# Performance work log

Hardware: AMD Instinct MI355X
Metric: run time of the kernel (lower is better)

The kernel has to match this reference:

```python
import jax, jax.numpy as jnp
import numpy as np

WS = 8  # window size (module uses window_sizes as a scalar)


def setup_inputs() -> dict:
    key = jax.random.key(0)
    ks = jax.random.split(key, 4)
    b, c, h, w = 4, 128, 256, 256
    x = jax.random.normal(ks[0], (b, c, h, w), jnp.float32)
    w_qkv = jax.random.normal(ks[1], (3 * c, c), jnp.float32) * (1.0 / np.sqrt(c))
    w_dw = jax.random.normal(ks[2], (3 * c, 1, 3, 3), jnp.float32) * (1.0 / 3.0)
    w_proj = jax.random.normal(ks[3], (c, c), jnp.float32) * (1.0 / np.sqrt(c))
    temperature = jnp.ones((1, 1, 1), jnp.float32)
    return {"x": x, "w_qkv": w_qkv, "w_dw": w_dw, "w_proj": w_proj,
            "temperature": temperature}


def _window(t, ws):
    # b c (h dh) (w dw) -> b (h w) (dh dw) c
    b, c, H, W = t.shape
    t = t.reshape(b, c, H // ws, ws, W // ws, ws)
    return t.transpose(0, 2, 4, 3, 5, 1).reshape(b, (H // ws) * (W // ws), ws * ws, c)


def _unwindow(t, ws, H, W):
    # b (h w) (dh dw) c -> b c (h dh) (w dw)
    b = t.shape[0]
    c = t.shape[-1]
    t = t.reshape(b, H // ws, W // ws, ws, ws, c)
    return t.transpose(0, 5, 1, 3, 2, 4).reshape(b, c, H, W)


def reference(x, w_qkv, w_dw, w_proj, temperature):
    b, c, H, W = x.shape
    ws = WS
    sh = -ws // 2  # = -(ws//2) for even ws, matching torch.roll shifts
    x_ = jnp.roll(x, (sh, sh), axis=(2, 3))
    # 1x1 conv c -> 3c
    qkv = jnp.einsum('oc,bchw->bohw', w_qkv, x_)
    # depthwise 3x3, padding 1
    qkv = jax.lax.conv_general_dilated(
        qkv, w_dw, window_strides=(1, 1), padding=[(1, 1), (1, 1)],
        dimension_numbers=('NCHW', 'OIHW', 'NCHW'), feature_group_count=3 * c)
    q, k, v = jnp.split(qkv, 3, axis=1)
    q = _window(q, ws)  # [b, nW, ws*ws, c]
    k = _window(k, ws)
    v = _window(v, ws)
    # L2-normalize along channel dim (torch F.normalize, eps=1e-12)
    q = q / jnp.maximum(jnp.linalg.norm(q, axis=-1, keepdims=True), 1e-12)
    k = k / jnp.maximum(jnp.linalg.norm(k, axis=-1, keepdims=True), 1e-12)
    # channel-wise attention: [b, nW, c, c]
    attn = jnp.einsum('bnpc,bnpd->bncd', q, k) * temperature.reshape(())
    attn = jax.nn.relu(attn)
    out = jnp.einsum('bnpc,bncd->bnpd', v, attn)  # [b, nW, ws*ws, c]
    out = _unwindow(out, ws, H, W)
    out = jnp.roll(out, (ws // 2, ws // 2), axis=(2, 3))
    y = jnp.einsum('oc,bchw->bohw', w_proj, out)
    return (y, attn)
```

## Files before the change

kernel.cpp:

```cpp
#include <hip/hip_runtime.h>
#include <hip/hip_bf16.h>

constexpr int NB = 4;
constexpr int CC = 128;
constexpr int HW = 65536;

using bf16x8 = __attribute__((ext_vector_type(8))) short;
using f32x4  = __attribute__((ext_vector_type(4))) float;

__device__ __forceinline__ unsigned short f2bf(float f) {
  unsigned u = __builtin_bit_cast(unsigned, f);
  u += 0x7FFFu + ((u >> 16) & 1u);
  return (unsigned short)(u >> 16);
}
__device__ __forceinline__ float bf2f(unsigned short s) {
  return __builtin_bit_cast(float, (unsigned)s << 16);
}

__device__ __forceinline__ void halo_decomp(int idx, int& ch, int& r, int& c) {
  ch = idx / 30;
  int rem = idx - ch * 30;
  r = rem / 3;
  c = rem - r * 3;
}
__device__ __forceinline__ uint4 halo_load_one(const __hip_bfloat16* __restrict__ base,
                                               int ih0, int iw0, int idx) {
  int ch, r, c;
  halo_decomp(idx, ch, r, c);
  int ii = ih0 - 1 + r, j0 = iw0 - 8 + c * 8;
  uint4 v = {0u, 0u, 0u, 0u};
  if ((unsigned)ii < 256u && (unsigned)j0 <= 248u)
    v = *(const uint4*)(base + (((size_t)ch) << 16) + (ii << 8) + j0);
  return v;
}
__device__ __forceinline__ void halo_store_one(unsigned short* __restrict__ halo,
                                               int idx, uint4 v) {
  int ch, r, c;
  halo_decomp(idx, ch, r, c);
  unsigned short* hrow = halo + ch * 168 + r * 16;
  if (c == 1) *(uint4*)hrow = v;
  else if (c == 0) hrow[9] = (unsigned short)(v.w >> 16);
  else hrow[8] = (unsigned short)(v.x & 0xFFFFu);
}

__device__ __forceinline__ void dw_row(const unsigned short* __restrict__ halo,
                                       const float* __restrict__ wd,
                                       int ch, int pr, float* __restrict__ outv) {
#pragma unroll
  for (int pc = 0; pc < 8; ++pc) outv[pc] = 0.f;
#pragma unroll
  for (int kr = 0; kr < 3; ++kr) {
    const unsigned short* hrow = halo + ch * 168 + (pr + kr) * 16;
    uint4 rw = *(const uint4*)hrow;
    float rv[10];
    rv[0] = bf2f((unsigned short)(rw.x & 0xFFFFu));
    rv[1] = bf2f((unsigned short)(rw.x >> 16));
    rv[2] = bf2f((unsigned short)(rw.y & 0xFFFFu));
    rv[3] = bf2f((unsigned short)(rw.y >> 16));
    rv[4] = bf2f((unsigned short)(rw.z & 0xFFFFu));
    rv[5] = bf2f((unsigned short)(rw.z >> 16));
    rv[6] = bf2f((unsigned short)(rw.w & 0xFFFFu));
    rv[7] = bf2f((unsigned short)(rw.w >> 16));
    rv[8] = bf2f(hrow[8]);
    rv[9] = bf2f(hrow[9]);
#pragma unroll
    for (int s = 0; s < 3; ++s) {
      float wv = wd[kr * 3 + s];
#pragma unroll
      for (int pc = 0; pc < 8; ++pc) {
        int m = pc + s - 1;
        float xv = (m < 0) ? rv[9] : rv[m];
        outv[pc] = fmaf(wv, xv, outv[pc]);
      }
    }
  }
}

__global__ __launch_bounds__(256) void k_qkv_mfma(const float* __restrict__ x,
                                                  const float* __restrict__ wq,
                                                  __hip_bfloat16* __restrict__ qkv) {
  __shared__ unsigned short x_s[128 * 136];

  int blk = blockIdx.x;
  int b = blk >> 9, i = (blk >> 1) & 255, jh = blk & 1;
  int j0 = jh << 7;
  int si = (i + 4) & 255;
  int t = threadIdx.x;

  {
    int c0 = (t & 63) << 1;
    int jb = (t >> 6) << 5;
    const float* xr0 = x + (((size_t)(b * CC + c0)) << 16) + (si << 8);
    const float* xr1 = xr0 + HW;
#pragma unroll
    for (int u = 0; u < 8; ++u) {
      int jj = jb + (u << 2);
      int sj = j0 + jj + 4;
      float v0[4], v1[4];
      if (sj + 3 <= 255) {
        *(float4*)v0 = *(const float4*)(xr0 + sj);
        *(float4*)v1 = *(const float4*)(xr1 + sj);
      } else {
#pragma unroll
        for (int e = 0; e < 4; ++e) {
          int s = (sj + e) & 255;
          v0[e] = xr0[s];
          v1[e] = xr1[s];
        }
      }
#pragma unroll
      for (int e = 0; e < 4; ++e) {
        unsigned pk = (unsigned)f2bf(v0[e]) | ((unsigned)f2bf(v1[e]) << 16);
        *(unsigned*)&x_s[(jj + e) * 136 + c0] = pk;
      }
    }
  }
  __syncthreads();

  int w = t >> 6;
  int lane = t & 63;
  int col = lane & 15;
  int kg = lane >> 4;

#pragma unroll 1
  for (int oi = 0; oi < 3; ++oi) {
    int m0 = oi * 128 + w * 32;
    bf16x8 afr[2][4];
#pragma unroll
    for (int mt = 0; mt < 2; ++mt) {
      const float* wr = wq + (m0 + mt * 16 + col) * CC + kg * 8;
#pragma unroll
      for (int ks = 0; ks < 4; ++ks) {
        float wa[4], wb[4];
        *(float4*)wa = *(const float4*)(wr + ks * 32);
        *(float4*)wb = *(const float4*)(wr + ks * 32 + 4);
        bf16x8 f;
#pragma unroll
        for (int e = 0; e < 4; ++e) {
          f[e] = (short)f2bf(wa[e]);
          f[e + 4] = (short)f2bf(wb[e]);
        }
        afr[mt][ks] = f;
      }
    }
#pragma unroll 1
    for (int n = 0; n < 8; ++n) {
      int px = n * 16 + col;
      f32x4 acc0 = {0.f, 0.f, 0.f, 0.f};
      f32x4 acc1 = {0.f, 0.f, 0.f, 0.f};
#pragma unroll
      for (int ks = 0; ks < 4; ++ks) {
        bf16x8 bfr = *(const bf16x8*)&x_s[px * 136 + ks * 32 + kg * 8];
        acc0 = __builtin_amdgcn_mfma_f32_16x16x32_bf16(afr[0][ks], bfr, acc0, 0, 0, 0);
        acc1 = __builtin_amdgcn_mfma_f32_16x16x32_bf16(afr[1][ks], bfr, acc1, 0, 0, 0);
      }
      int j = j0 + n * 16 + col;
#pragma unroll
      for (int r = 0; r < 4; ++r) {
        int och0 = m0 + kg * 4 + r;
        int och1 = m0 + 16 + kg * 4 + r;
        int g0 = och0 >> 7, c0 = och0 & 127;
        int g1 = och1 >> 7, c1 = och1 & 127;
        qkv[(((size_t)((g0 * NB + b) * CC + c0)) << 16) + (i << 8) + j] =
            __float2bfloat16(acc0[r]);
        qkv[(((size_t)((g1 * NB + b) * CC + c1)) << 16) + (i << 8) + j] =
            __float2bfloat16(acc1[r]);
      }
    }
  }
}

__global__ __launch_bounds__(256) void k_attn(const __hip_bfloat16* __restrict__ qkv,
                                              const float* __restrict__ wdw,
                                              const float* __restrict__ temp_p,
                                              float* __restrict__ attn_out) {
  __shared__ unsigned short halo_s[128 * 168];
  __shared__ unsigned short q_t[128][72];
  __shared__ unsigned short k_t[128][72];
  __shared__ float sumsq_s[2][64];

  int blk = blockIdx.x;
  int b = blk >> 10, n = blk & 1023;
  int ih0 = (n >> 5) << 3, iw0 = (n & 31) << 3;
  int t = threadIdx.x;
  int ch_l = t & 15, grp = t >> 4;
  int pr = grp & 7, contrib = grp >> 3;
  float tau = temp_p[0];
  const __hip_bfloat16* qbase = qkv + (((size_t)(b * CC)) << 16);
  const __hip_bfloat16* kbase = qkv + (((size_t)((NB + b) * CC)) << 16);

#pragma unroll
  for (int it = 0; it < 15; ++it) {
    int idx = it * 256 + t;
    halo_store_one(halo_s, idx, halo_load_one(qbase, ih0, iw0, idx));
  }
  __syncthreads();

  uint4 kpre[15];
#pragma unroll
  for (int it = 0; it < 15; ++it)
    kpre[it] = halo_load_one(kbase, ih0, iw0, it * 256 + t);

  float outv[4][8];
  float ssq[8];
#pragma unroll
  for (int pc = 0; pc < 8; ++pc) ssq[pc] = 0.f;
#pragma unroll
  for (int it = 0; it < 4; ++it) {
    int ch = ((contrib + 2 * it) << 4) + ch_l;
    float wd[9];
#pragma unroll
    for (int kk = 0; kk < 9; ++kk) wd[kk] = wdw[ch * 9 + kk];
    dw_row(halo_s, wd, ch, pr, outv[it]);
#pragma unroll
    for (int pc = 0; pc < 8; ++pc) ssq[pc] = fmaf(outv[it][pc], outv[it][pc], ssq[pc]);
  }
#pragma unroll
  for (int pc = 0; pc < 8; ++pc) {
    float s = ssq[pc];
    s += __shfl_xor(s, 1);
    s += __shfl_xor(s, 2);
    s += __shfl_xor(s, 4);
    s += __shfl_xor(s, 8);
    ssq[pc] = s;
  }
  if (ch_l == 0) {
#pragma unroll
    for (int pc = 0; pc < 8; ++pc) sumsq_s[contrib][pr * 8 + pc] = ssq[pc];
  }
  __syncthreads();

#pragma unroll
  for (int it = 0; it < 15; ++it) halo_store_one(halo_s, it * 256 + t, kpre[it]);

  {
    float psv[8];
#pragma unroll
    for (int pc = 0; pc < 8; ++pc) {
      float s = sumsq_s[0][pr * 8 + pc] + sumsq_s[1][pr * 8 + pc];
      psv[pc] = 1.f / fmaxf(sqrtf(s), 1e-12f);
    }
#pragma unroll
    for (int it = 0; it < 4; ++it) {
      int ch = ((contrib + 2 * it) << 4) + ch_l;
      unsigned short o8[8];
#pragma unroll
      for (int pc = 0; pc < 8; ++pc) o8[pc] = f2bf(outv[it][pc] * psv[pc]);
      *(uint4*)&q_t[ch][pr * 8] = *(const uint4*)o8;
    }
  }
  __syncthreads();

#pragma unroll
  for (int pc = 0; pc < 8; ++pc) ssq[pc] = 0.f;
#pragma unroll
  for (int it = 0; it < 4; ++it) {
    int ch = ((contrib + 2 * it) << 4) + ch_l;
    float wd[9];
#pragma unroll
    for (int kk = 0; kk < 9; ++kk) wd[kk] = wdw[(CC + ch) * 9 + kk];
    dw_row(halo_s, wd, ch, pr, outv[it]);
#pragma unroll
    for (int pc = 0; pc < 8; ++pc) ssq[pc] = fmaf(outv[it][pc], outv[it][pc], ssq[pc]);
  }
#pragma unroll
  for (int pc = 0; pc < 8; ++pc) {
    float s = ssq[pc];
    s += __shfl_xor(s, 1);
    s += __shfl_xor(s, 2);
    s += __shfl_xor(s, 4);
    s += __shfl_xor(s, 8);
    ssq[pc] = s;
  }
  if (ch_l == 0) {
#pragma unroll
    for (int pc = 0; pc < 8; ++pc) sumsq_s[contrib][pr * 8 + pc] = ssq[pc];
  }
  __syncthreads();

  {
    float psv[8];
#pragma unroll
    for (int pc = 0; pc < 8; ++pc) {
      float s = sumsq_s[0][pr * 8 + pc] + sumsq_s[1][pr * 8 + pc];
      psv[pc] = tau / fmaxf(sqrtf(s), 1e-12f);
    }
#pragma unroll
    for (int it = 0; it < 4; ++it) {
      int ch = ((contrib + 2 * it) << 4) + ch_l;
      unsigned short o8[8];
#pragma unroll
      for (int pc = 0; pc < 8; ++pc) o8[pc] = f2bf(outv[it][pc] * psv[pc]);
      *(uint4*)&k_t[ch][pr * 8] = *(const uint4*)o8;
    }
  }
  __syncthreads();

  int wv = t >> 6, lane = t & 63;
  int col = lane & 15, kg = lane >> 4;
  int c0 = wv * 32;
  bf16x8 afr[2][2];
#pragma unroll
  for (int mt = 0; mt < 2; ++mt)
#pragma unroll
    for (int ks = 0; ks < 2; ++ks)
      afr[mt][ks] = *(const bf16x8*)&q_t[c0 + mt * 16 + col][ks * 32 + kg * 8];
  float* ao = attn_out + ((size_t)blk << 14);
#pragma unroll
  for (int dt = 0; dt < 8; ++dt) {
    bf16x8 b0 = *(const bf16x8*)&k_t[dt * 16 + col][kg * 8];
    bf16x8 b1 = *(const bf16x8*)&k_t[dt * 16 + col][32 + kg * 8];
    f32x4 a0 = {0.f, 0.f, 0.f, 0.f};
    f32x4 a1 = {0.f, 0.f, 0.f, 0.f};
    a0 = __builtin_amdgcn_mfma_f32_16x16x32_bf16(afr[0][0], b0, a0, 0, 0, 0);
    a0 = __builtin_amdgcn_mfma_f32_16x16x32_bf16(afr[0][1], b1, a0, 0, 0, 0);
    a1 = __builtin_amdgcn_mfma_f32_16x16x32_bf16(afr[1][0], b0, a1, 0, 0, 0);
    a1 = __builtin_amdgcn_mfma_f32_16x16x32_bf16(afr[1][1], b1, a1, 0, 0, 0);
#pragma unroll
    for (int r = 0; r < 4; ++r) {
      ao[((c0 + kg * 4 + r) << 7) + dt * 16 + col] = fmaxf(a0[r], 0.f);
      ao[((c0 + 16 + kg * 4 + r) << 7) + dt * 16 + col] = fmaxf(a1[r], 0.f);
    }
  }
}

__device__ __forceinline__ int at_addr(int d, int cbyte) {
  int a = d * 272 + cbyte;
  return a ^ (((d >> 2) & 7) << 4);
}

__global__ __launch_bounds__(256) void k_pv(const __hip_bfloat16* __restrict__ qkv,
                                            const float* __restrict__ wdw,
                                            const float* __restrict__ attn,
                                            __hip_bfloat16* __restrict__ out_win) {
  __shared__ unsigned short halo_s[128 * 168];
  __shared__ unsigned short v_t[64][136];

  int blk = blockIdx.x;
  int b = blk >> 10, n = blk & 1023;
  int ih0 = (n >> 5) << 3, iw0 = (n & 31) << 3;
  int t = threadIdx.x;
  int ch_l = t & 15, grp = t >> 4;
  int pr = grp & 7, contrib = grp >> 3;
  const __hip_bfloat16* vbase = qkv + (((size_t)((2 * NB + b) * CC)) << 16);

#pragma unroll
  for (int it = 0; it < 15; ++it) {
    int idx = it * 256 + t;
    halo_store_one(halo_s, idx, halo_load_one(vbase, ih0, iw0, idx));
  }
  __syncthreads();

  const float* ab = attn + ((size_t)blk << 14);
  float4 apre[8][2];
#pragma unroll
  for (int it = 0; it < 8; ++it) {
    int idx = it * 256 + t;
    int d4 = idx & 31, cp = idx >> 5;
    const float* ar = ab + ((2 * cp) << 7) + 4 * d4;
    apre[it][0] = *(const float4*)ar;
    apre[it][1] = *(const float4*)(ar + 128);
  }

#pragma unroll
  for (int it = 0; it < 4; ++it) {
    int ch = ((contrib + 2 * it) << 4) + ch_l;
    float wd[9];
#pragma unroll
    for (int kk = 0; kk < 9; ++kk) wd[kk] = wdw[(2 * CC + ch) * 9 + kk];
    float outv[8];
    dw_row(halo_s, wd, ch, pr, outv);
#pragma unroll
    for (int pc = 0; pc < 8; ++pc) v_t[pr * 8 + pc][ch] = f2bf(outv[pc]);
  }
  __syncthreads();

  unsigned short* a_t = halo_s;
#pragma unroll
  for (int it = 0; it < 8; ++it) {
    int idx = it * 256 + t;
    int d4 = idx & 31, cp = idx >> 5;
    float lo[4], hi[4];
    *(float4*)lo = apre[it][0];
    *(float4*)hi = apre[it][1];
#pragma unroll
    for (int e = 0; e < 4; ++e) {
      unsigned pk = (unsigned)f2bf(lo[e]) | ((unsigned)f2bf(hi[e]) << 16);
      *(unsigned*)((char*)a_t + at_addr(4 * d4 + e, 4 * cp)) = pk;
    }
  }
  __syncthreads();

  int wv = t >> 6, lane = t & 63;
  int col = lane & 15, kg = lane >> 4;
  f32x4 acc[8];
#pragma unroll
  for (int dt = 0; dt < 8; ++dt) acc[dt] = {0.f, 0.f, 0.f, 0.f};
#pragma unroll
  for (int ks = 0; ks < 4; ++ks) {
    bf16x8 va = *(const bf16x8*)&v_t[wv * 16 + col][ks * 32 + kg * 8];
#pragma unroll
    for (int dt = 0; dt < 8; ++dt) {
      bf16x8 bf = *(const bf16x8*)((const char*)a_t +
                                   at_addr(dt * 16 + col, (ks * 32 + kg * 8) * 2));
      acc[dt] = __builtin_amdgcn_mfma_f32_16x16x32_bf16(va, bf, acc[dt], 0, 0, 0);
    }
  }
  __hip_bfloat16* ow = out_win + ((size_t)blk << 13);
#pragma unroll
  for (int dt = 0; dt < 8; ++dt)
#pragma unroll
    for (int r = 0; r < 4; ++r)
      ow[((wv * 16 + kg * 4 + r) << 7) + dt * 16 + col] = __float2bfloat16(acc[dt][r]);
}

__global__ __launch_bounds__(256) void k_proj_mfma(const __hip_bfloat16* __restrict__ out_win,
                                                   const float* __restrict__ wp,
                                                   float* __restrict__ y) {
  __shared__ unsigned short w_s[128 * 136];

  int t = threadIdx.x;
  {
    int och = t >> 1, ch0 = (t & 1) << 6;
    const float* wr = wp + och * CC + ch0;
#pragma unroll
    for (int u = 0; u < 32; ++u) {
      float2 v = *(const float2*)(wr + 2 * u);
      unsigned pk = (unsigned)f2bf(v.x) | ((unsigned)f2bf(v.y) << 16);
      *(unsigned*)&w_s[och * 136 + ch0 + 2 * u] = pk;
    }
  }
  __syncthreads();

  int w = t >> 6, lane = t & 63;
  int col = lane & 15, kg = lane >> 4;
  int bn = blockIdx.x * 4 + w;
  int b = bn >> 10, n = bn & 1023;
  const __hip_bfloat16* ob = out_win + ((size_t)bn << 13);

  bf16x8 afr[8][4];
#pragma unroll
  for (int mt = 0; mt < 8; ++mt)
#pragma unroll
    for (int ks = 0; ks < 4; ++ks)
      afr[mt][ks] = *(const bf16x8*)&w_s[(mt * 16 + col) * 136 + ks * 32 + kg * 8];

#pragma unroll 1
  for (int nt = 0; nt < 4; ++nt) {
    int p = nt * 16 + col;
    bf16x8 bfr[4];
#pragma unroll
    for (int ks = 0; ks < 4; ++ks)
      bfr[ks] = *(const bf16x8*)(ob + p * CC + ks * 32 + kg * 8);
    int i_f = (((n >> 5) << 3) + (p >> 3) + 4) & 255;
    int j_f = (((n & 31) << 3) + (p & 7) + 4) & 255;
    float* yp = y + (((size_t)b * CC) << 16) + (i_f << 8) + j_f;
#pragma unroll
    for (int mt = 0; mt < 8; ++mt) {
      f32x4 acc = {0.f, 0.f, 0.f, 0.f};
#pragma unroll
      for (int ks = 0; ks < 4; ++ks)
        acc = __builtin_amdgcn_mfma_f32_16x16x32_bf16(afr[mt][ks], bfr[ks], acc, 0, 0, 0);
#pragma unroll
      for (int r = 0; r < 4; ++r) {
        int och = mt * 16 + kg * 4 + r;
        yp[(size_t)och << 16] = acc[r];
      }
    }
  }
}

extern "C" void kernel_launch(void* const* d_in, const int* in_sizes, int n_in,
                              void* d_out, int out_size, void* d_ws, size_t ws_size,
                              hipStream_t stream) {
  const float* x = (const float*)d_in[0];
  const float* w_qkv = (const float*)d_in[1];
  const float* w_dw = (const float*)d_in[2];
  const float* w_proj = (const float*)d_in[3];
  const float* temp = (const float*)d_in[4];
  float* y = (float*)d_out;
  float* attn = (float*)d_out + (size_t)NB * CC * HW;

  __hip_bfloat16* qkv = (__hip_bfloat16*)d_ws;
  __hip_bfloat16* out_win = (__hip_bfloat16*)d_ws;

  k_qkv_mfma<<<2048, 256, 0, stream>>>(x, w_qkv, qkv);
  k_attn<<<4096, 256, 0, stream>>>(qkv, w_dw, temp, attn);
  k_pv<<<4096, 256, 0, stream>>>(qkv, w_dw, attn, out_win);
  k_proj_mfma<<<1024, 256, 0, stream>>>(out_win, w_proj, y);
}
```

Measured before the change: 676.8 us.

## Fuse attention, PV and projection kernels into one per-window kernel

Merges k_attn, k_pv and k_proj_mfma into a single kernel. The ReLU'd attention matrix stays in registers and goes to LDS for the PV matmul, instead of being written to global memory and read back. The windowed output also stays in LDS for the projection, which removes the out_win round trip and two kernel launches. The projection weights are now read from global memory and converted to bf16 per block rather than staged once per block in LDS. The change also adds a block-index remap and a launch_bounds occupancy hint, and raises register pressure because the attention accumulators and prefetched V stay live.

```diff
diff --git a/kernel.cpp b/kernel.cpp
--- a/kernel.cpp
+++ b/kernel.cpp
@@ -170,16 +170,19 @@
   }
 }
 
-__global__ __launch_bounds__(256) void k_attn(const __hip_bfloat16* __restrict__ qkv,
-                                              const float* __restrict__ wdw,
-                                              const float* __restrict__ temp_p,
-                                              float* __restrict__ attn_out) {
+__global__ __launch_bounds__(256, 2) void k_fused(const __hip_bfloat16* __restrict__ qkv,
+                                                  const float* __restrict__ wdw,
+                                                  const float* __restrict__ temp_p,
+                                                  const float* __restrict__ wp,
+                                                  float* __restrict__ attn_out,
+                                                  float* __restrict__ y) {
   __shared__ unsigned short halo_s[128 * 168];
   __shared__ unsigned short q_t[128][72];
   __shared__ unsigned short k_t[128][72];
   __shared__ float sumsq_s[2][64];
 
-  int blk = blockIdx.x;
+  int bid = blockIdx.x;
+  int blk = ((bid & 7) << 9) + (bid >> 3);
   int b = blk >> 10, n = blk & 1023;
   int ih0 = (n >> 5) << 3, iw0 = (n & 31) << 3;
   int t = threadIdx.x;
@@ -188,6 +191,7 @@
   float tau = temp_p[0];
   const __hip_bfloat16* qbase = qkv + (((size_t)(b * CC)) << 16);
   const __hip_bfloat16* kbase = qkv + (((size_t)((NB + b) * CC)) << 16);
+  const __hip_bfloat16* vbase = qkv + (((size_t)((2 * NB + b) * CC)) << 16);
 
 #pragma unroll
   for (int it = 0; it < 15; ++it) {
@@ -232,7 +236,6 @@
 
 #pragma unroll
   for (int it = 0; it < 15; ++it) halo_store_one(halo_s, it * 256 + t, kpre[it]);
-
   {
     float psv[8];
 #pragma unroll
@@ -296,171 +299,126 @@
   }
   __syncthreads();
 
+  uint4 vpre[15];
+#pragma unroll
+  for (int it = 0; it < 15; ++it)
+    vpre[it] = halo_load_one(vbase, ih0, iw0, it * 256 + t);
+
   int wv = t >> 6, lane = t & 63;
   int col = lane & 15, kg = lane >> 4;
   int c0 = wv * 32;
-  bf16x8 afr[2][2];
-#pragma unroll
-  for (int mt = 0; mt < 2; ++mt)
-#pragma unroll
-    for (int ks = 0; ks < 2; ++ks)
-      afr[mt][ks] = *(const bf16x8*)&q_t[c0 + mt * 16 + col][ks * 32 + kg * 8];
-  float* ao = attn_out + ((size_t)blk << 14);
-#pragma unroll
-  for (int dt = 0; dt < 8; ++dt) {
-    bf16x8 b0 = *(const bf16x8*)&k_t[dt * 16 + col][kg * 8];
-    bf16x8 b1 = *(const bf16x8*)&k_t[dt * 16 + col][32 + kg * 8];
-    f32x4 a0 = {0.f, 0.f, 0.f, 0.f};
-    f32x4 a1 = {0.f, 0.f, 0.f, 0.f};
-    a0 = __builtin_amdgcn_mfma_f32_16x16x32_bf16(afr[0][0], b0, a0, 0, 0, 0);
-    a0 = __builtin_amdgcn_mfma_f32_16x16x32_bf16(afr[0][1], b1, a0, 0, 0, 0);
-    a1 = __builtin_amdgcn_mfma_f32_16x16x32_bf16(afr[1][0], b0, a1, 0, 0, 0);
-    a1 = __builtin_amdgcn_mfma_f32_16x16x32_bf16(afr[1][1], b1, a1, 0, 0, 0);
-#pragma unroll
-    for (int r = 0; r < 4; ++r) {
-      ao[((c0 + kg * 4 + r) << 7) + dt * 16 + col] = fmaxf(a0[r], 0.f);
-      ao[((c0 + 16 + kg * 4 + r) << 7) + dt * 16 + col] = fmaxf(a1[r], 0.f);
-    }
-  }
-}
-
-__device__ __forceinline__ int at_addr(int d, int cbyte) {
-  int a = d * 272 + cbyte;
-  return a ^ (((d >> 2) & 7) << 4);
-}
-
-__global__ __launch_bounds__(256) void k_pv(const __hip_bfloat16* __restrict__ qkv,
-                                            const float* __restrict__ wdw,
-                                            const float* __restrict__ attn,
-                                            __hip_bfloat16* __restrict__ out_win) {
-  __shared__ unsigned short halo_s[128 * 168];
-  __shared__ unsigned short v_t[64][136];
-
-  int blk = blockIdx.x;
-  int b = blk >> 10, n = blk & 1023;
-  int ih0 = (n >> 5) << 3, iw0 = (n & 31) << 3;
-  int t = threadIdx.x;
-  int ch_l = t & 15, grp = t >> 4;
-  int pr = grp & 7, contrib = grp >> 3;
-  const __hip_bfloat16* vbase = qkv + (((size_t)((2 * NB + b) * CC)) << 16);
-
-#pragma unroll
-  for (int it = 0; it < 15; ++it) {
-    int idx = it * 256 + t;
-    halo_store_one(halo_s, idx, halo_load_one(vbase, ih0, iw0, idx));
-  }
-  __syncthreads();
-
-  const float* ab = attn + ((size_t)blk << 14);
-  float4 apre[8][2];
-#pragma unroll
-  for (int it = 0; it < 8; ++it) {
-    int idx = it * 256 + t;
-    int d4 = idx & 31, cp = idx >> 5;
-    const float* ar = ab + ((2 * cp) << 7) + 4 * d4;
-    apre[it][0] = *(const float4*)ar;
-    apre[it][1] = *(const float4*)(ar + 128);
-  }
-
+  f32x4 pa0[8], pa1[8];
+  {
+    bf16x8 afr[2][2];
+#pragma unroll
+    for (int mt = 0; mt < 2; ++mt)
+#pragma unroll
+      for (int ks = 0; ks < 2; ++ks)
+        afr[mt][ks] = *(const bf16x8*)&q_t[c0 + mt * 16 + col][ks * 32 + kg * 8];
+    float* ao = attn_out + ((size_t)blk << 14);
+#pragma unroll
+    for (int dt = 0; dt < 8; ++dt) {
+      bf16x8 b0 = *(const bf16x8*)&k_t[dt * 16 + col][kg * 8];
+      bf16x8 b1 = *(const bf16x8*)&k_t[dt * 16 + col][32 + kg * 8];
+      f32x4 a0 = {0.f, 0.f, 0.f, 0.f};
+      f32x4 a1 = {0.f, 0.f, 0.f, 0.f};
+      a0 = __builtin_amdgcn_mfma_f32_16x16x32_bf16(afr[0][0], b0, a0, 0, 0, 0);
+      a0 = __builtin_amdgcn_mfma_f32_16x16x32_bf16(afr[0][1], b1, a0, 0, 0, 0);
+      a1 = __builtin_amdgcn_mfma_f32_16x16x32_bf16(afr[1][0], b0, a1, 0, 0, 0);
+      a1 = __builtin_amdgcn_mfma_f32_16x16x32_bf16(afr[1][1], b1, a1, 0, 0, 0);
+#pragma unroll
+      for (int r = 0; r < 4; ++r) {
+        a0[r] = fmaxf(a0[r], 0.f);
+        a1[r] = fmaxf(a1[r], 0.f);
+        ao[((c0 + kg * 4 + r) << 7) + dt * 16 + col] = a0[r];
+        ao[((c0 + 16 + kg * 4 + r) << 7) + dt * 16 + col] = a1[r];
+      }
+      pa0[dt] = a0;
+      pa1[dt] = a1;
+    }
+  }
+  __syncthreads();
+
+#pragma unroll
+  for (int it = 0; it < 15; ++it) halo_store_one(halo_s, it * 256 + t, vpre[it]);
+  __syncthreads();
+
+  unsigned short (*v_t)[136] = (unsigned short (*)[136])&q_t[0][0];
 #pragma unroll
   for (int it = 0; it < 4; ++it) {
     int ch = ((contrib + 2 * it) << 4) + ch_l;
     float wd[9];
 #pragma unroll
     for (int kk = 0; kk < 9; ++kk) wd[kk] = wdw[(2 * CC + ch) * 9 + kk];
-    float outv[8];
-    dw_row(halo_s, wd, ch, pr, outv);
-#pragma unroll
-    for (int pc = 0; pc < 8; ++pc) v_t[pr * 8 + pc][ch] = f2bf(outv[pc]);
-  }
-  __syncthreads();
-
-  unsigned short* a_t = halo_s;
-#pragma unroll
-  for (int it = 0; it < 8; ++it) {
-    int idx = it * 256 + t;
-    int d4 = idx & 31, cp = idx >> 5;
-    float lo[4], hi[4];
-    *(float4*)lo = apre[it][0];
-    *(float4*)hi = apre[it][1];
-#pragma unroll
-    for (int e = 0; e < 4; ++e) {
-      unsigned pk = (unsigned)f2bf(lo[e]) | ((unsigned)f2bf(hi[e]) << 16);
-      *(unsigned*)((char*)a_t + at_addr(4 * d4 + e, 4 * cp)) = pk;
-    }
-  }
-  __syncthreads();
-
-  int wv = t >> 6, lane = t & 63;
-  int col = lane & 15, kg = lane >> 4;
-  f32x4 acc[8];
-#pragma unroll
-  for (int dt = 0; dt < 8; ++dt) acc[dt] = {0.f, 0.f, 0.f, 0.f};
+    float vo[8];
+    dw_row(halo_s, wd, ch, pr, vo);
+#pragma unroll
+    for (int pc = 0; pc < 8; ++pc) v_t[pr * 8 + pc][ch] = f2bf(vo[pc]);
+  }
+  __syncthreads();
+
+  unsigned short (*a_t)[136] = (unsigned short (*)[136])halo_s;
+#pragma unroll
+  for (int dt = 0; dt < 8; ++dt)
+#pragma unroll
+    for (int r = 0; r < 4; ++r) {
+      a_t[dt * 16 + col][c0 + kg * 4 + r] = f2bf(pa0[dt][r]);
+      a_t[dt * 16 + col][c0 + 16 + kg * 4 + r] = f2bf(pa1[dt][r]);
+    }
+  __syncthreads();
+
+  f32x4 pacc[8];
+#pragma unroll
+  for (int dt = 0; dt < 8; ++dt) pacc[dt] = {0.f, 0.f, 0.f, 0.f};
 #pragma unroll
   for (int ks = 0; ks < 4; ++ks) {
     bf16x8 va = *(const bf16x8*)&v_t[wv * 16 + col][ks * 32 + kg * 8];
 #pragma unroll
     for (int dt = 0; dt < 8; ++dt) {
-      bf16x8 bf = *(const bf16x8*)((const char*)a_t +
-                                   at_addr(dt * 16 + col, (ks * 32 + kg * 8) * 2));
-      acc[dt] = __builtin_amdgcn_mfma_f32_16x16x32_bf16(va, bf, acc[dt], 0, 0, 0);
-    }
-  }
-  __hip_bfloat16* ow = out_win + ((size_t)blk << 13);
+      bf16x8 bf = *(const bf16x8*)&a_t[dt * 16 + col][ks * 32 + kg * 8];
+      pacc[dt] = __builtin_amdgcn_mfma_f32_16x16x32_bf16(va, bf, pacc[dt], 0, 0, 0);
+    }
+  }
+  __syncthreads();
+
+  unsigned short (*po_t)[136] = (unsigned short (*)[136])halo_s;
 #pragma unroll
   for (int dt = 0; dt < 8; ++dt)
 #pragma unroll
     for (int r = 0; r < 4; ++r)
-      ow[((wv * 16 + kg * 4 + r) << 7) + dt * 16 + col] = __float2bfloat16(acc[dt][r]);
-}
-
-__global__ __launch_bounds__(256) void k_proj_mfma(const __hip_bfloat16* __restrict__ out_win,
-                                                   const float* __restrict__ wp,
-                                                   float* __restrict__ y) {
-  __shared__ unsigned short w_s[128 * 136];
-
-  int t = threadIdx.x;
+      po_t[wv * 16 + kg * 4 + r][dt * 16 + col] = f2bf(pacc[dt][r]);
+  __syncthreads();
+
   {
-    int och = t >> 1, ch0 = (t & 1) << 6;
-    const float* wr = wp + och * CC + ch0;
-#pragma unroll
-    for (int u = 0; u < 32; ++u) {
-      float2 v = *(const float2*)(wr + 2 * u);
-      unsigned pk = (unsigned)f2bf(v.x) | ((unsigned)f2bf(v.y) << 16);
-      *(unsigned*)&w_s[och * 136 + ch0 + 2 * u] = pk;
-    }
-  }
-  __syncthreads();
-
-  int w = t >> 6, lane = t & 63;
-  int col = lane & 15, kg = lane >> 4;
-  int bn = blockIdx.x * 4 + w;
-  int b = bn >> 10, n = bn & 1023;
-  const __hip_bfloat16* ob = out_win + ((size_t)bn << 13);
-
-  bf16x8 afr[8][4];
-#pragma unroll
-  for (int mt = 0; mt < 8; ++mt)
+    int p = wv * 16 + col;
+    bf16x8 bfr[4];
 #pragma unroll
     for (int ks = 0; ks < 4; ++ks)
-      afr[mt][ks] = *(const bf16x8*)&w_s[(mt * 16 + col) * 136 + ks * 32 + kg * 8];
-
-#pragma unroll 1
-  for (int nt = 0; nt < 4; ++nt) {
-    int p = nt * 16 + col;
-    bf16x8 bfr[4];
-#pragma unroll
-    for (int ks = 0; ks < 4; ++ks)
-      bfr[ks] = *(const bf16x8*)(ob + p * CC + ks * 32 + kg * 8);
+      bfr[ks] = *(const bf16x8*)&po_t[p][ks * 32 + kg * 8];
     int i_f = (((n >> 5) << 3) + (p >> 3) + 4) & 255;
     int j_f = (((n & 31) << 3) + (p & 7) + 4) & 255;
     float* yp = y + (((size_t)b * CC) << 16) + (i_f << 8) + j_f;
 #pragma unroll
     for (int mt = 0; mt < 8; ++mt) {
+      bf16x8 afr[4];
+      const float* wr = wp + (mt * 16 + col) * CC + kg * 8;
+#pragma unroll
+      for (int ks = 0; ks < 4; ++ks) {
+        float wa[4], wb[4];
+        *(float4*)wa = *(const float4*)(wr + ks * 32);
+        *(float4*)wb = *(const float4*)(wr + ks * 32 + 4);
+        bf16x8 f;
+#pragma unroll
+        for (int e = 0; e < 4; ++e) {
+          f[e] = (short)f2bf(wa[e]);
+          f[e + 4] = (short)f2bf(wb[e]);
+        }
+        afr[ks] = f;
+      }
       f32x4 acc = {0.f, 0.f, 0.f, 0.f};
 #pragma unroll
       for (int ks = 0; ks < 4; ++ks)
-        acc = __builtin_amdgcn_mfma_f32_16x16x32_bf16(afr[mt][ks], bfr[ks], acc, 0, 0, 0);
+        acc = __builtin_amdgcn_mfma_f32_16x16x32_bf16(afr[ks], bfr[ks], acc, 0, 0, 0);
 #pragma unroll
       for (int r = 0; r < 4; ++r) {
         int och = mt * 16 + kg * 4 + r;
@@ -482,10 +440,7 @@
   float* attn = (float*)d_out + (size_t)NB * CC * HW;
 
   __hip_bfloat16* qkv = (__hip_bfloat16*)d_ws;
-  __hip_bfloat16* out_win = (__hip_bfloat16*)d_ws;
 
   k_qkv_mfma<<<2048, 256, 0, stream>>>(x, w_qkv, qkv);
-  k_attn<<<4096, 256, 0, stream>>>(qkv, w_dw, temp, attn);
-  k_pv<<<4096, 256, 0, stream>>>(qkv, w_dw, attn, out_win);
-  k_proj_mfma<<<1024, 256, 0, stream>>>(out_win, w_proj, y);
-}
+  k_fused<<<4096, 256, 0, stream>>>(qkv, w_dw, temp, w_proj, attn, y);
+}
```

New measurement: 646.6 us. 1.05x faster.
